# Kernel optimization log

Measured on AMD Instinct MI355X. Metric: run time of the kernel, lower is better.

Reference implementation:

```python
import jax, jax.numpy as jnp
import numpy as np

B = 32          # graphs per batch
NPG = 512       # nodes per graph
EPG = 2048      # original edges per graph (stored in y[:, -1])
N = B * NPG     # 16384 nodes
E = B * EPG     # 65536 edges
GF = 5          # num_global_features
ETOT = E + N    # edges after add_self_loops

def _lin(k, o, i):
    return jax.random.normal(k, (o, i), jnp.float32) / np.sqrt(i)

def setup_inputs():
    key = jax.random.key(0)
    ks = jax.random.split(key, 20)
    x = jax.random.normal(ks[0], (N,), jnp.float32)
    off = (jnp.arange(B, dtype=jnp.int32) * NPG)[:, None]
    src = (jax.random.randint(ks[1], (B, EPG), 0, NPG, dtype=jnp.int32) + off).reshape(-1)
    dst = (jax.random.randint(ks[2], (B, EPG), 0, NPG, dtype=jnp.int32) + off).reshape(-1)
    edge_index = jnp.stack([src, dst])
    edge_attr = jax.random.normal(ks[3], (E, GF), jnp.float32)
    # last global feature = number of edges per graph (module reads y[:, -1])
    y = jax.random.normal(ks[4], (B, GF), jnp.float32).at[:, -1].set(float(EPG)).reshape(-1)
    batch_vector = jnp.repeat(jnp.arange(B, dtype=jnp.int32), NPG)
    p = dict(
        Wn=_lin(ks[5], 512, 1), bn=jnp.zeros(512, jnp.float32),
        We=_lin(ks[6], 511, GF), be=jnp.zeros(511, jnp.float32),
        Wg=_lin(ks[7], 512, GF), bg=jnp.zeros(512, jnp.float32),
        Wl=_lin(ks[8], 1024, 512), bl=jnp.zeros(1024, jnp.float32),
        Wr=_lin(ks[9], 1024, 512), br=jnp.zeros(1024, jnp.float32),
        Wge=_lin(ks[10], 1024, 511),
        att=jax.random.normal(ks[11], (1024,), jnp.float32) / 32.0,
        bgat=jnp.zeros(1024, jnp.float32),
        Wm=_lin(ks[12], 1024, 1024), bm=jnp.zeros(1024, jnp.float32),
        Wmi=_lin(ks[13], 1024, 1024), bmi=jnp.zeros(1024, jnp.float32),
        Wce=_lin(ks[14], 1024, 512), bce=jnp.zeros(1024, jnp.float32),
        W1=_lin(ks[15], 256, 2048), b1=jnp.zeros(256, jnp.float32),
        W2=_lin(ks[16], 1, 256), b2=jnp.zeros(1, jnp.float32),
    )
    return dict(x=x, edge_index=edge_index, edge_attr=edge_attr, y=y,
                batch_vector=batch_vector, **p)

def _leaky(v, s=0.01):
    return jnp.where(v >= 0, v, s * v)

def _forward(edge_index, batch_vector, x, edge_attr, y, Wn, bn, We, be, Wg, bg,
             Wl, bl, Wr, br, Wge, att, bgat, Wm, bm, Wmi, bmi, Wce, bce,
             W1, b1, W2, b2):
    # add_self_loops (fill_value=1.0 for edge_attr), self loops appended last
    loops = jnp.arange(N, dtype=edge_index.dtype)
    src = jnp.concatenate([edge_index[0], loops])
    dst = jnp.concatenate([edge_index[1], loops])
    ea = jnp.concatenate([edge_attr, jnp.ones((N, GF), edge_attr.dtype)], axis=0)
    # preprocessing MLPs (dropout = identity at inference)
    h = _leaky(x[:, None] @ Wn.T + bn)               # [N, 512]
    e = _leaky(ea @ We.T + be)                       # [ETOT, 511]
    yg = _leaky(y.reshape(B, GF) @ Wg.T + bg)        # [B, 512]
    # GATv2Conv, 1 head, concat, negative_slope=0.2, no self-loop add
    xl = h @ Wl.T + bl                               # source transform [N, 1024]
    xr = h @ Wr.T + br                               # target transform [N, 1024]
    m = _leaky(xl[src] + xr[dst] + e @ Wge.T, 0.2)   # [ETOT, 1024]
    logit = m @ att                                  # [ETOT]
    mx = jax.ops.segment_max(logit, dst, num_segments=N)
    ex = jnp.exp(logit - mx[dst])
    alpha = ex / (jax.ops.segment_sum(ex, dst, num_segments=N)[dst] + 1e-16)
    gat = jax.ops.segment_sum(alpha[:, None] * xl[src], dst, num_segments=N) + bgat
    edge_total = jnp.concatenate([e, alpha[:, None]], axis=1)  # [ETOT, 512]
    # GeneralConv: undirected message, add aggregation, identity skip (in==out)
    hm = gat @ Wm.T + bm
    hmi = gat @ Wmi.T + bmi
    eh = edge_total @ Wce.T + bce                    # [ETOT, 1024]
    deg = jax.ops.segment_sum(jnp.ones((ETOT,), gat.dtype), dst, num_segments=N)
    conv = (jax.ops.segment_sum(hm[src] + eh, dst, num_segments=N)
            + deg[:, None] * hmi + gat)              # [N, 1024]
    # global mean pooling (nodes) and module's contiguous edge batch vector
    nc = jax.ops.segment_sum(jnp.ones((N,), conv.dtype), batch_vector, num_segments=B)
    pn = jax.ops.segment_sum(conv, batch_vector, num_segments=B) / nc[:, None]
    ebatch = jnp.repeat(jnp.arange(B, dtype=jnp.int32), EPG + NPG)
    pe = jax.ops.segment_sum(edge_total, ebatch, num_segments=B) / float(EPG + NPG)
    pooled = jnp.concatenate([pn, pe, yg], axis=1)   # [B, 2048]
    out = _leaky(pooled @ W1.T + b1) @ W2.T + b2
    return jax.nn.sigmoid(out)                       # [B, 1]

def reference(x, edge_index, edge_attr, y, batch_vector, Wn, bn, We, be, Wg, bg,
              Wl, bl, Wr, br, Wge, att, bgat, Wm, bm, Wmi, bmi, Wce, bce,
              W1, b1, W2, b2):
    return _forward(edge_index, batch_vector, x, edge_attr, y, Wn, bn, We, be,
                    Wg, bg, Wl, bl, Wr, br, Wge, att, bgat, Wm, bm, Wmi, bmi,
                    Wce, bce, W1, b1, W2, b2)
```

## Files before the change

### kernel.cpp

```cpp
#include <hip/hip_runtime.h>
#include <cstdint>
#include <cstddef>

#define N_NODES 16384
#define N_EDGES 65536
#define ETOT    81920
#define B_GR    32

typedef __attribute__((ext_vector_type(8))) short bf16x8;
typedef __attribute__((ext_vector_type(4))) float f32x4;

static constexpr size_t OFF_XL    = 0;
static constexpr size_t OFF_XR    = 33554432ULL;
static constexpr size_t OFF_EBF   = 67108864ULL;
static constexpr size_t OFF_HBF   = 67108864ULL;
static constexpr size_t OFF_WCAT  = 83886080ULL;
static constexpr size_t OFF_ROWP  = 67108864ULL;
static constexpr size_t OFF_CSR   = 67174656ULL;
static constexpr size_t OFF_ALPHA = 67502336ULL;
static constexpr size_t OFF_WGEP  = 134217728ULL;
static constexpr size_t OFF_LPART = 135266304ULL;
static constexpr size_t OFF_DEG   = 137363456ULL;
static constexpr size_t OFF_ODEG  = 137428992ULL;
static constexpr size_t OFF_CURS  = 137494528ULL;
static constexpr size_t OFF_PG    = 137560064ULL;
static constexpr size_t OFF_PDG   = 137691136ULL;
static constexpr size_t OFF_PGAT  = 137822208ULL;
static constexpr size_t OFF_PS    = 137953280ULL;
static constexpr size_t OFF_PE    = 138018816ULL;
static constexpr size_t OFF_WLOOP = 138084352ULL;
static constexpr size_t OFF_YG    = 138088448ULL;
static constexpr size_t OFF_PN    = 138153984ULL;

__device__ __forceinline__ float leaky01(float v){ return v >= 0.f ? v : 0.01f*v; }
__device__ __forceinline__ float leaky02(float v){ return v >= 0.f ? v : 0.2f*v; }
__device__ __forceinline__ unsigned short f2bf(float f){
  union { float f; unsigned u; } v; v.f = f;
  unsigned r = v.u + 0x7FFFu + ((v.u >> 16) & 1u);
  return (unsigned short)(r >> 16);
}
__device__ __forceinline__ float bf2f(unsigned short h){
  union { unsigned u; float f; } v; v.u = ((unsigned)h) << 16;
  return v.f;
}

__global__ __launch_bounds__(256) void k_prep0(
    const float* __restrict__ x, const float* __restrict__ Wn, const float* __restrict__ bn,
    const float* __restrict__ Wl, const float* __restrict__ Wr,
    const float* __restrict__ Wge, const float* __restrict__ y,
    const float* __restrict__ Wg, const float* __restrict__ bg,
    const float* __restrict__ We, const float* __restrict__ be,
    float* __restrict__ zone, unsigned short* __restrict__ h_bf,
    unsigned short* __restrict__ Wcat, unsigned short* __restrict__ Wge_p,
    float* __restrict__ yg, float* __restrict__ we_loop) {
  __shared__ float e_lds[512];
  int bx = blockIdx.x, tid = threadIdx.x;
  if (bx < 176) {
    ((float4*)zone)[bx*256 + tid] = (float4){0.f,0.f,0.f,0.f};
  } else if (bx < 1200) {
    int gid = (bx-176)*256 + tid;
    int base = gid*8;
    int n = base >> 9, j = base & 511;
    float xv = x[n];
    float4 w0 = *(const float4*)(Wn + j);
    float4 w1 = *(const float4*)(Wn + j + 4);
    float4 b0 = *(const float4*)(bn + j);
    float4 b1 = *(const float4*)(bn + j + 4);
    unsigned short o[8];
    o[0]=f2bf(leaky01(xv*w0.x+b0.x)); o[1]=f2bf(leaky01(xv*w0.y+b0.y));
    o[2]=f2bf(leaky01(xv*w0.z+b0.z)); o[3]=f2bf(leaky01(xv*w0.w+b0.w));
    o[4]=f2bf(leaky01(xv*w1.x+b1.x)); o[5]=f2bf(leaky01(xv*w1.y+b1.y));
    o[6]=f2bf(leaky01(xv*w1.z+b1.z)); o[7]=f2bf(leaky01(xv*w1.w+b1.w));
    ((uint4*)h_bf)[gid] = *(const uint4*)o;
  } else if (bx < 2224) {
    int i = (bx-1200)*256 + tid;
    int base = i*4;
    const float* src = (base < 524288) ? (Wl + base) : (Wr + base - 524288);
    float4 v = *(const float4*)src;
    ushort4 o; o.x=f2bf(v.x); o.y=f2bf(v.y); o.z=f2bf(v.z); o.w=f2bf(v.w);
    ((ushort4*)Wcat)[i] = o;
  } else if (bx < 4272) {
    int gid = (bx-2224)*256 + tid;
    int j = gid >> 9, k = gid & 511;
    Wge_p[gid] = (k < 511) ? f2bf(Wge[(size_t)j*511 + k]) : (unsigned short)0;
  } else if (bx < 4336) {
    int gid = (bx-4272)*256 + tid;
    int b = gid >> 9, j = gid & 511;
    float s = bg[j];
    #pragma unroll
    for (int k=0;k<5;k++) s += y[b*5+k]*Wg[j*5+k];
    yg[gid] = leaky01(s);
  } else {
    for (int c = tid; c < 512; c += 256) {
      float v = 0.f;
      if (c < 511) {
        float s = be[c];
        #pragma unroll
        for (int q=0;q<5;q++) s += We[c*5+q];
        v = leaky01(s);
      }
      e_lds[c] = v;
    }
    __syncthreads();
    int j = (bx-4336)*256 + tid;
    float s = 0.f;
    for (int k=0;k<511;k++) s += e_lds[k]*Wge[(size_t)j*511+k];
    we_loop[j] = s;
  }
}

__global__ __launch_bounds__(256) void k_prep_e(
    const float* __restrict__ ea, const float* __restrict__ We, const float* __restrict__ be,
    unsigned short* __restrict__ E_bf) {
  int gid = blockIdx.x*256 + threadIdx.x;
  int e = gid >> 6, cg = gid & 63;
  int c0 = cg*8;
  const float* e5 = ea + (size_t)e*5;
  float a0=e5[0], a1=e5[1], a2=e5[2], a3=e5[3], a4=e5[4];
  unsigned short o[8];
  #pragma unroll
  for (int j=0;j<8;j++) {
    int c = c0 + j;
    float v = 0.f;
    if (c < 511) {
      const float* w = We + c*5;
      float s = be[c] + a0*w[0] + a1*w[1] + a2*w[2] + a3*w[3] + a4*w[4];
      v = leaky01(s);
    }
    o[j] = f2bf(v);
  }
  ((uint4*)E_bf)[gid] = *(const uint4*)o;
}

__global__ void k_deg(const int* __restrict__ ei, int* __restrict__ deg, int* __restrict__ odeg) {
  int i = blockIdx.x*blockDim.x + threadIdx.x;
  int s, d;
  if (i < N_EDGES) { s = ei[i]; d = ei[N_EDGES + i]; }
  else { s = i - N_EDGES; d = s; }
  atomicAdd(&deg[d], 1);
  atomicAdd(&odeg[s], 1);
}

__global__ __launch_bounds__(1024) void k_scan(const int* __restrict__ deg, int* __restrict__ rowptr) {
  __shared__ int sums[1024];
  int t = threadIdx.x;
  int local[16]; int s = 0;
  #pragma unroll
  for (int i=0;i<16;i++){ local[i] = deg[t*16+i]; s += local[i]; }
  sums[t] = s; __syncthreads();
  for (int off=1; off<1024; off<<=1) {
    int v = (t >= off) ? sums[t-off] : 0;
    __syncthreads();
    sums[t] += v;
    __syncthreads();
  }
  int run = (t==0) ? 0 : sums[t-1];
  if (t==0) rowptr[0] = 0;
  #pragma unroll
  for (int i=0;i<16;i++){ run += local[i]; rowptr[t*16+i+1] = run; }
}

__global__ void k_fill_csr(const int* __restrict__ ei, const int* __restrict__ rowptr,
                           int* __restrict__ cursor, int* __restrict__ csr) {
  int i = blockIdx.x*blockDim.x + threadIdx.x;
  int d = (i < N_EDGES) ? ei[N_EDGES + i] : (i - N_EDGES);
  int pos = rowptr[d] + atomicAdd(&cursor[d], 1);
  csr[pos] = i;
}


__global__ __launch_bounds__(256) void k_gemm_xlxr(
    const unsigned short* __restrict__ h_bf, const unsigned short* __restrict__ Wcat,
    const float* __restrict__ bl, const float* __restrict__ br,
    unsigned short* __restrict__ xl_bf, unsigned short* __restrict__ xr_bf) {
  __shared__ unsigned short As[2][4096];
  __shared__ unsigned short Bs[2][4096];
  int blk = blockIdx.x;
  int xcd = blk & 7, slot = blk >> 3;
  int bx = xcd*16 + (slot >> 4), by = slot & 15;
  int row0 = bx*128, col0 = by*128;
  int tid = threadIdx.x;
  int w = tid >> 6, lane = tid & 63;
  int wm = w >> 1, wn = w & 1;
  int quad = lane >> 4, l16 = lane & 15;
  int ldoff = w*512 + lane*8;
  const unsigned short* gA = h_bf + (size_t)(row0 + w*16 + l16)*512 + quad*8;
  const unsigned short* gB = Wcat + (size_t)(col0 + w*16 + l16)*512 + quad*8;
  f32x4 acc[4][4];
  #pragma unroll
  for (int i=0;i<4;i++)
    #pragma unroll
    for (int j=0;j<4;j++) acc[i][j] = (f32x4){0.f,0.f,0.f,0.f};

  {
    uint4 a0 = *(const uint4*)(gA);
    uint4 a1 = *(const uint4*)(gA + 32768);
    uint4 b0 = *(const uint4*)(gB);
    uint4 b1 = *(const uint4*)(gB + 32768);
    *(uint4*)&As[0][ldoff] = a0; *(uint4*)&As[0][2048+ldoff] = a1;
    *(uint4*)&Bs[0][ldoff] = b0; *(uint4*)&Bs[0][2048+ldoff] = b1;
  }
  __syncthreads();
  int cur = 0;
  #pragma unroll 2
  for (int k0 = 32; k0 <= 512; k0 += 32) {
    uint4 na0, na1, nb0, nb1;
    bool more = (k0 < 512);
    if (more) {
      na0 = *(const uint4*)(gA + k0);
      na1 = *(const uint4*)(gA + 32768 + k0);
      nb0 = *(const uint4*)(gB + k0);
      nb1 = *(const uint4*)(gB + 32768 + k0);
    }
    bf16x8 af[4], bfr[4];
    #pragma unroll
    for (int mi=0;mi<4;mi++)
      af[mi] = *(const bf16x8*)&As[cur][(wm*4+mi)*512 + quad*128 + l16*8];
    #pragma unroll
    for (int ni=0;ni<4;ni++)
      bfr[ni] = *(const bf16x8*)&Bs[cur][(wn*4+ni)*512 + quad*128 + l16*8];
    #pragma unroll
    for (int mi=0;mi<4;mi++)
      #pragma unroll
      for (int ni=0;ni<4;ni++)
        acc[mi][ni] = __builtin_amdgcn_mfma_f32_16x16x32_bf16(af[mi], bfr[ni], acc[mi][ni], 0, 0, 0);
    if (more) {
      *(uint4*)&As[cur^1][ldoff] = na0; *(uint4*)&As[cur^1][2048+ldoff] = na1;
      *(uint4*)&Bs[cur^1][ldoff] = nb0; *(uint4*)&Bs[cur^1][2048+ldoff] = nb1;
    }
    __syncthreads();
    cur ^= 1;
  }
  bool isL = (by < 8);
  const float* bias = isL ? bl : br;
  unsigned short* O = isL ? xl_bf : xr_bf;
  int cb = isL ? col0 : (col0 - 1024);
  float bias4[4];
  #pragma unroll
  for (int ni=0;ni<4;ni++) bias4[ni] = bias[cb + wn*64 + ni*16 + l16];
  #pragma unroll
  for (int mi=0;mi<4;mi++)
    #pragma unroll
    for (int ni=0;ni<4;ni++) {
      int col = cb + wn*64 + ni*16 + l16;
      #pragma unroll
      for (int r=0;r<4;r++) {
        int row = row0 + wm*64 + mi*16 + quad*4 + r;
        O[(size_t)row*1024 + col] = f2bf(acc[mi][ni][r] + bias4[ni]);
      }
    }
}

__global__ __launch_bounds__(256) void k_mfma_we(
    const unsigned short* __restrict__ E_bf, const unsigned short* __restrict__ Wge_bf,
    const int* __restrict__ ei,
    const unsigned short* __restrict__ xl_bf, const unsigned short* __restrict__ xr_bf,
    const float* __restrict__ att, float* __restrict__ logit_part) {
  __shared__ unsigned short As[2][4096];
  __shared__ unsigned short Bs[2][4096];
  __shared__ float tmp[128];
  int blk = blockIdx.x;
  int xcd = blk & 7, slot = blk >> 3;
  int bx = xcd*64 + (slot >> 3), by = slot & 7;
  int row0 = bx*128, col0 = by*128;
  int tid = threadIdx.x;
  int w = tid >> 6, lane = tid & 63;
  int wm = w >> 1, wn = w & 1;
  int quad = lane >> 4, l16 = lane & 15;
  int ldoff = w*512 + lane*8;
  const unsigned short* gA = E_bf  + (size_t)(row0 + w*16 + l16)*512 + quad*8;
  const unsigned short* gB = Wge_bf + (size_t)(col0 + w*16 + l16)*512 + quad*8;
  f32x4 acc[4][4];
  #pragma unroll
  for (int i=0;i<4;i++)
    #pragma unroll
    for (int j=0;j<4;j++) acc[i][j] = (f32x4){0.f,0.f,0.f,0.f};

  {
    uint4 a0 = *(const uint4*)(gA);
    uint4 a1 = *(const uint4*)(gA + 32768);
    uint4 b0 = *(const uint4*)(gB);
    uint4 b1 = *(const uint4*)(gB + 32768);
    *(uint4*)&As[0][ldoff] = a0; *(uint4*)&As[0][2048+ldoff] = a1;
    *(uint4*)&Bs[0][ldoff] = b0; *(uint4*)&Bs[0][2048+ldoff] = b1;
  }
  __syncthreads();
  int cur = 0;
  #pragma unroll 2
  for (int k0 = 32; k0 <= 512; k0 += 32) {
    uint4 na0, na1, nb0, nb1;
    bool more = (k0 < 512);
    if (more) {
      na0 = *(const uint4*)(gA + k0);
      na1 = *(const uint4*)(gA + 32768 + k0);
      nb0 = *(const uint4*)(gB + k0);
      nb1 = *(const uint4*)(gB + 32768 + k0);
    }
    bf16x8 af[4], bfr[4];
    #pragma unroll
    for (int mi=0;mi<4;mi++)
      af[mi] = *(const bf16x8*)&As[cur][(wm*4+mi)*512 + quad*128 + l16*8];
    #pragma unroll
    for (int ni=0;ni<4;ni++)
      bfr[ni] = *(const bf16x8*)&Bs[cur][(wn*4+ni)*512 + quad*128 + l16*8];
    #pragma unroll
    for (int mi=0;mi<4;mi++)
      #pragma unroll
      for (int ni=0;ni<4;ni++)
        acc[mi][ni] = __builtin_amdgcn_mfma_f32_16x16x32_bf16(af[mi], bfr[ni], acc[mi][ni], 0, 0, 0);
    if (more) {
      *(uint4*)&As[cur^1][ldoff] = na0; *(uint4*)&As[cur^1][2048+ldoff] = na1;
      *(uint4*)&Bs[cur^1][ldoff] = nb0; *(uint4*)&Bs[cur^1][2048+ldoff] = nb1;
    }
    __syncthreads();
    cur ^= 1;
  }
  float att4[4];
  #pragma unroll
  for (int ni=0;ni<4;ni++) att4[ni] = att[col0 + wn*64 + ni*16 + l16];
  float pv[4][4];
  #pragma unroll
  for (int mi=0;mi<4;mi++) {
    #pragma unroll
    for (int r=0;r<4;r++) {
      int e = row0 + wm*64 + mi*16 + quad*4 + r;
      int s = ei[e], d = ei[N_EDGES + e];
      const unsigned short* xlr = xl_bf + (size_t)s*1024;
      const unsigned short* xrr = xr_bf + (size_t)d*1024;
      float p = 0.f;
      #pragma unroll
      for (int ni=0;ni<4;ni++) {
        int col = col0 + wn*64 + ni*16 + l16;
        float z = acc[mi][ni][r] + bf2f(xlr[col]) + bf2f(xrr[col]);
        z = leaky02(z);
        p += z*att4[ni];
      }
      p += __shfl_down(p, 8, 16);
      p += __shfl_down(p, 4, 16);
      p += __shfl_down(p, 2, 16);
      p += __shfl_down(p, 1, 16);
      pv[mi][r] = p;
    }
  }
  if (wn == 1 && l16 == 0) {
    #pragma unroll
    for (int mi=0;mi<4;mi++)
      #pragma unroll
      for (int r=0;r<4;r++)
        tmp[wm*64 + mi*16 + quad*4 + r] = pv[mi][r];
  }
  __syncthreads();
  if (wn == 0 && l16 == 0) {
    #pragma unroll
    for (int mi=0;mi<4;mi++)
      #pragma unroll
      for (int r=0;r<4;r++) {
        int le = wm*64 + mi*16 + quad*4 + r;
        logit_part[(size_t)(row0 + le)*8 + by] = pv[mi][r] + tmp[le];
      }
  }
}

__global__ __launch_bounds__(256) void k_softmax_gat(
    const int* __restrict__ ei, const int* __restrict__ rowptr, const int* __restrict__ csr,
    const float* __restrict__ logit_part,
    const unsigned short* __restrict__ xl_bf, const unsigned short* __restrict__ xr_bf,
    const float* __restrict__ we_loop, const float* __restrict__ att,
    const float* __restrict__ bgat,
    float* __restrict__ alpha, unsigned short* __restrict__ gat_bf) {
  __shared__ float sl[256];
  __shared__ int   se[256];
  __shared__ float red[256];
  int blk = blockIdx.x;
  int n = ((blk & 7) << 11) + (blk >> 3);
  int tid = threadIdx.x;
  {
    ushort4 a = ((const ushort4*)(xl_bf + (size_t)n*1024))[tid];
    ushort4 b = ((const ushort4*)(xr_bf + (size_t)n*1024))[tid];
    float4 c = ((const float4*)we_loop)[tid];
    float4 t = ((const float4*)att)[tid];
    float s = 0.f;
    s += leaky02(bf2f(a.x)+bf2f(b.x)+c.x)*t.x;
    s += leaky02(bf2f(a.y)+bf2f(b.y)+c.y)*t.y;
    s += leaky02(bf2f(a.z)+bf2f(b.z)+c.z)*t.z;
    s += leaky02(bf2f(a.w)+bf2f(b.w)+c.w)*t.w;
    red[tid] = s;
  }
  __syncthreads();
  #pragma unroll
  for (int off=128; off; off>>=1){ if (tid<off) red[tid] += red[tid+off]; __syncthreads(); }
  float sll = red[0];
  __syncthreads();

  int beg = rowptr[n], end = rowptr[n+1], cnt = end - beg;
  float m = -1e30f;
  for (int p = beg+tid; p < end; p += 256) {
    int e = csr[p];
    float lg;
    if (e < N_EDGES) {
      const float4* lp = (const float4*)(logit_part + (size_t)e*8);
      float4 q0 = lp[0], q1 = lp[1];
      lg = q0.x+q0.y+q0.z+q0.w+q1.x+q1.y+q1.z+q1.w;
    } else lg = sll;
    int idx = p - beg;
    if (idx < 256) { se[idx] = e; sl[idx] = lg; }
    m = fmaxf(m, lg);
  }
  red[tid] = m; __syncthreads();
  #pragma unroll
  for (int off=128; off; off>>=1){ if (tid<off) red[tid] = fmaxf(red[tid], red[tid+off]); __syncthreads(); }
  m = red[0];
  __syncthreads();
  float ss = 0.f;
  for (int p = beg+tid; p < end; p += 256) {
    int idx = p - beg;
    ss += expf(sl[idx] - m);
  }
  red[tid] = ss; __syncthreads();
  #pragma unroll
  for (int off=128; off; off>>=1){ if (tid<off) red[tid] += red[tid+off]; __syncthreads(); }
  float inv = 1.f/(red[0] + 1e-16f);
  __syncthreads();
  for (int p = beg+tid; p < end; p += 256) {
    int idx = p - beg;
    float a = expf(sl[idx] - m)*inv;
    alpha[se[idx]] = a;
    sl[idx] = a;
  }
  __syncthreads();
  float4 acc = ((const float4*)bgat)[tid];
  for (int p = 0; p < cnt; p++) {
    float a = sl[p]; int e = se[p];
    int s = (e < N_EDGES) ? ei[e] : (e - N_EDGES);
    ushort4 v = ((const ushort4*)(xl_bf + (size_t)s*1024))[tid];
    acc.x += a*bf2f(v.x); acc.y += a*bf2f(v.y); acc.z += a*bf2f(v.z); acc.w += a*bf2f(v.w);
  }
  ushort4 o; o.x=f2bf(acc.x); o.y=f2bf(acc.y); o.z=f2bf(acc.z); o.w=f2bf(acc.w);
  ((ushort4*)(gat_bf + (size_t)n*1024))[tid] = o;
}

__global__ __launch_bounds__(256) void k_nodepool(
    const unsigned short* __restrict__ gat_bf, const int* __restrict__ odeg,
    const int* __restrict__ rowptr,
    float* __restrict__ P_G, float* __restrict__ P_DG, float* __restrict__ P_gat) {
  int b = blockIdx.x, yy = blockIdx.y;
  int nc = yy >> 2, cg = yy & 3;
  int col = cg*256 + threadIdx.x;
  float a1=0.f, a2=0.f, a3=0.f;
  int n0 = b*512 + nc*128;
  for (int i=0;i<128;i++){
    int n = n0 + i;
    float g = bf2f(gat_bf[(size_t)n*1024 + col]);
    float od = (float)odeg[n];
    float dg = (float)(rowptr[n+1]-rowptr[n]);
    a1 += od*g; a2 += dg*g; a3 += g;
  }
  atomicAdd(&P_G[b*1024+col], a1);
  atomicAdd(&P_DG[b*1024+col], a2);
  atomicAdd(&P_gat[b*1024+col], a3);
}

__global__ __launch_bounds__(256) void k_edgepool(
    const float* __restrict__ ea, const float* __restrict__ We, const float* __restrict__ be,
    const float* __restrict__ alpha, float* __restrict__ P_S, float* __restrict__ pe) {
  __shared__ float sea[640];
  __shared__ float sal[128];
  int b = blockIdx.x, chy = blockIdx.y, tid = threadIdx.x;
  int mode = (chy < 20) ? 0 : 1;
  int ch = (chy < 20) ? chy : (chy - 20);
  int c1 = tid, c2 = tid + 256;
  bool v2 = (c2 < 511);
  float w1[5], w2[5]={0,0,0,0,0}, b1v, b2v=0.f;
  #pragma unroll
  for (int q=0;q<5;q++) w1[q] = We[c1*5+q];
  b1v = be[c1];
  if (v2) {
    #pragma unroll
    for (int q=0;q<5;q++) w2[q] = We[c2*5+q];
    b2v = be[c2];
  }
  int base = (mode == 0)
    ? ((ch < 16) ? (b*2048 + ch*128) : (N_EDGES + b*512 + (ch-16)*128))
    : (b*2560 + ch*128);
  for (int i=tid;i<640;i+=256){
    int r = base + i/5;
    sea[i] = (r < N_EDGES) ? ea[(size_t)r*5 + (i%5)] : 1.0f;
  }
  for (int i=tid;i<128;i+=256) sal[i] = alpha[base + i];
  __syncthreads();
  float acc1 = 0.f, acc2 = 0.f;
  for (int rr=0; rr<128; rr++) {
    const float* er = &sea[rr*5];
    acc1 += leaky01(b1v + er[0]*w1[0]+er[1]*w1[1]+er[2]*w1[2]+er[3]*w1[3]+er[4]*w1[4]);
    if (v2) acc2 += leaky01(b2v + er[0]*w2[0]+er[1]*w2[1]+er[2]*w2[2]+er[3]*w2[3]+er[4]*w2[4]);
    else    acc2 += sal[rr];
  }
  if (mode == 0) {
    atomicAdd(&P_S[b*512+c1], acc1);
    atomicAdd(&P_S[b*512+c2], acc2);
  } else {
    const float sc = 1.f/2560.f;
    atomicAdd(&pe[b*512+c1], acc1*sc);
    atomicAdd(&pe[b*512+c2], acc2*sc);
  }
}

__global__ __launch_bounds__(256) void k_pn(
    const float* __restrict__ P_G, const float* __restrict__ P_DG,
    const float* __restrict__ P_S, const float* __restrict__ P_gat,
    const float* __restrict__ Wm, const float* __restrict__ bm,
    const float* __restrict__ Wmi, const float* __restrict__ bmi,
    const float* __restrict__ Wce, const float* __restrict__ bce,
    float* __restrict__ pn) {
  __shared__ float sPg[1024], sPdg[1024], sPs[512];
  int b = blockIdx.x, col0 = blockIdx.y*64;
  int tid = threadIdx.x, w = tid >> 6, lane = tid & 63;
  for (int i=tid;i<1024;i+=256){ sPg[i]=P_G[b*1024+i]; sPdg[i]=P_DG[b*1024+i]; }
  for (int i=tid;i<512;i+=256) sPs[i]=P_S[b*512+i];
  __syncthreads();
  for (int c=0;c<16;c++){
    int j = col0 + w*16 + c;
    const float* wm  = Wm  + (size_t)j*1024;
    const float* wmi = Wmi + (size_t)j*1024;
    const float* wce = Wce + (size_t)j*512;
    float s = 0.f;
    #pragma unroll 4
    for (int i=0;i<16;i++){ int k = lane + i*64; s += sPg[k]*wm[k] + sPdg[k]*wmi[k]; }
    #pragma unroll 4
    for (int i=0;i<8;i++){ int k = lane + i*64; s += sPs[k]*wce[k]; }
    #pragma unroll
    for (int off=32; off; off>>=1) s += __shfl_down(s, off);
    if (lane == 0) {
      pn[b*1024+j] = (s + P_gat[b*1024+j] + 2560.f*(bm[j]+bmi[j]+bce[j])) * (1.f/512.f);
    }
  }
}

__global__ __launch_bounds__(256) void k_final(
    const float* __restrict__ pn, const float* __restrict__ pe, const float* __restrict__ yg,
    const float* __restrict__ W1, const float* __restrict__ b1,
    const float* __restrict__ W2, const float* __restrict__ b2,
    float* __restrict__ out) {
  __shared__ float pooled[2048];
  __shared__ float red[256];
  int b = blockIdx.x, tid = threadIdx.x;
  for (int i=tid;i<1024;i+=256) pooled[i]      = pn[b*1024+i];
  for (int i=tid;i<512;i+=256)  pooled[1024+i] = pe[b*512+i];
  for (int i=tid;i<512;i+=256)  pooled[1536+i] = yg[b*512+i];
  __syncthreads();
  const float4* w4 = (const float4*)(W1 + (size_t)tid*2048);
  const float4* p4 = (const float4*)pooled;
  float s = b1[tid];
  for (int k=0;k<512;k++){
    float4 w = w4[k]; float4 p = p4[k];
    s += w.x*p.x + w.y*p.y + w.z*p.z + w.w*p.w;
  }
  s = leaky01(s);
  red[tid] = s * W2[tid];
  __syncthreads();
  for (int off=128; off; off>>=1){
    if (tid < off) red[tid] += red[tid+off];
    __syncthreads();
  }
  if (tid == 0){
    float o = red[0] + b2[0];
    out[b] = 1.f/(1.f+expf(-o));
  }
}

extern "C" void kernel_launch(void* const* d_in, const int* in_sizes, int n_in,
                              void* d_out, int out_size, void* d_ws, size_t ws_size,
                              hipStream_t stream) {
  const float* x   = (const float*)d_in[0];
  const int*   ei  = (const int*)  d_in[1];
  const float* ea  = (const float*)d_in[2];
  const float* y   = (const float*)d_in[3];
  const float* Wn  = (const float*)d_in[5];
  const float* bn  = (const float*)d_in[6];
  const float* We  = (const float*)d_in[7];
  const float* be  = (const float*)d_in[8];
  const float* Wg  = (const float*)d_in[9];
  const float* bg  = (const float*)d_in[10];
  const float* Wl  = (const float*)d_in[11];
  const float* bl  = (const float*)d_in[12];
  const float* Wr  = (const float*)d_in[13];
  const float* br  = (const float*)d_in[14];
  const float* Wge = (const float*)d_in[15];
  const float* att = (const float*)d_in[16];
  const float* bgat= (const float*)d_in[17];
  const float* Wm  = (const float*)d_in[18];
  const float* bm  = (const float*)d_in[19];
  const float* Wmi = (const float*)d_in[20];
  const float* bmi = (const float*)d_in[21];
  const float* Wce = (const float*)d_in[22];
  const float* bce = (const float*)d_in[23];
  const float* W1  = (const float*)d_in[24];
  const float* b1  = (const float*)d_in[25];
  const float* W2  = (const float*)d_in[26];
  const float* b2  = (const float*)d_in[27];
  float* out = (float*)d_out;

  char* ws = (char*)d_ws;
  unsigned short* xl_bf  = (unsigned short*)(ws + OFF_XL);
  unsigned short* xr_bf  = (unsigned short*)(ws + OFF_XR);
  unsigned short* gat_bf = (unsigned short*)(ws + OFF_XR);
  unsigned short* E_bf   = (unsigned short*)(ws + OFF_EBF);
  unsigned short* h_bf   = (unsigned short*)(ws + OFF_HBF);
  unsigned short* Wcat   = (unsigned short*)(ws + OFF_WCAT);
  unsigned short* Wge_p  = (unsigned short*)(ws + OFF_WGEP);
  float* lpart  = (float*)(ws + OFF_LPART);
  float* zone   = (float*)(ws + OFF_DEG);
  int*   deg    = (int*)  (ws + OFF_DEG);
  int*   odeg   = (int*)  (ws + OFF_ODEG);
  int*   cursor = (int*)  (ws + OFF_CURS);
  float* P_G    = (float*)(ws + OFF_PG);
  float* P_DG   = (float*)(ws + OFF_PDG);
  float* P_gat  = (float*)(ws + OFF_PGAT);
  float* P_S    = (float*)(ws + OFF_PS);
  float* pe     = (float*)(ws + OFF_PE);
  int*   rowptr = (int*)  (ws + OFF_ROWP);
  int*   csr    = (int*)  (ws + OFF_CSR);
  float* alpha  = (float*)(ws + OFF_ALPHA);
  float* we_loop= (float*)(ws + OFF_WLOOP);
  float* yg     = (float*)(ws + OFF_YG);
  float* pn     = (float*)(ws + OFF_PN);

  k_prep0<<<dim3(4340), dim3(256), 0, stream>>>(x, Wn, bn, Wl, Wr, Wge, y, Wg, bg, We, be,
                                                zone, h_bf, Wcat, Wge_p, yg, we_loop);
  k_gemm_xlxr<<<dim3(2048), dim3(256), 0, stream>>>(h_bf, Wcat, bl, br, xl_bf, xr_bf);
  k_prep_e<<<dim3(16384), dim3(256), 0, stream>>>(ea, We, be, E_bf);
  k_mfma_we<<<dim3(4096), dim3(256), 0, stream>>>(E_bf, Wge_p, ei, xl_bf, xr_bf, att, lpart);
  k_deg<<<dim3(320), dim3(256), 0, stream>>>(ei, deg, odeg);
  k_scan<<<dim3(1), dim3(1024), 0, stream>>>(deg, rowptr);
  k_fill_csr<<<dim3(320), dim3(256), 0, stream>>>(ei, rowptr, cursor, csr);
  k_softmax_gat<<<dim3(16384), dim3(256), 0, stream>>>(ei, rowptr, csr, lpart, xl_bf, xr_bf,
                                                       we_loop, att, bgat, alpha, gat_bf);
  k_nodepool<<<dim3(32,16), dim3(256), 0, stream>>>(gat_bf, odeg, rowptr, P_G, P_DG, P_gat);
  k_edgepool<<<dim3(32,40), dim3(256), 0, stream>>>(ea, We, be, alpha, P_S, pe);
  k_pn<<<dim3(32,16), dim3(256), 0, stream>>>(P_G, P_DG, P_S, P_gat, Wm, bm, Wmi, bmi, Wce, bce, pn);
  k_final<<<dim3(32), dim3(256), 0, stream>>>(pn, pe, yg, W1, b1, W2, b2, out);
}
```

Measured before the change: 617.2 us.

## Load GEMM B operands directly from global and transpose epilogue through LDS

In both MFMA GEMM kernels the weight (B) tile is no longer staged through shared memory. Each wave instead loads its bf16 fragments straight from global memory, relying on the cache since the weights are shared across blocks. This halves LDS use and drops the B shared-memory stores. In k_mfma_we, the attention-logit epilogue now writes the accumulators to LDS in transposed form. Four threads per edge can then read contiguous 32-column spans of xl/xr with 16-byte vector loads instead of scattered 2-byte gathers. The trade-off is unstaged global loads of B inside the inner loop and extra LDS traffic and barriers in the epilogue.

```diff
diff --git a/kernel.cpp b/kernel.cpp
--- a/kernel.cpp
+++ b/kernel.cpp
@@ -174,7 +174,6 @@
     const float* __restrict__ bl, const float* __restrict__ br,
     unsigned short* __restrict__ xl_bf, unsigned short* __restrict__ xr_bf) {
   __shared__ unsigned short As[2][4096];
-  __shared__ unsigned short Bs[2][4096];
   int blk = blockIdx.x;
   int xcd = blk & 7, slot = blk >> 3;
   int bx = xcd*16 + (slot >> 4), by = slot & 15;
@@ -185,7 +184,7 @@
   int quad = lane >> 4, l16 = lane & 15;
   int ldoff = w*512 + lane*8;
   const unsigned short* gA = h_bf + (size_t)(row0 + w*16 + l16)*512 + quad*8;
-  const unsigned short* gB = Wcat + (size_t)(col0 + w*16 + l16)*512 + quad*8;
+  const unsigned short* gB = Wcat + (size_t)(col0 + wn*64 + l16)*512 + quad*8;
   f32x4 acc[4][4];
   #pragma unroll
   for (int i=0;i<4;i++)
@@ -195,30 +194,26 @@
   {
     uint4 a0 = *(const uint4*)(gA);
     uint4 a1 = *(const uint4*)(gA + 32768);
-    uint4 b0 = *(const uint4*)(gB);
-    uint4 b1 = *(const uint4*)(gB + 32768);
     *(uint4*)&As[0][ldoff] = a0; *(uint4*)&As[0][2048+ldoff] = a1;
-    *(uint4*)&Bs[0][ldoff] = b0; *(uint4*)&Bs[0][2048+ldoff] = b1;
   }
   __syncthreads();
   int cur = 0;
   #pragma unroll 2
   for (int k0 = 32; k0 <= 512; k0 += 32) {
-    uint4 na0, na1, nb0, nb1;
+    uint4 na0, na1;
     bool more = (k0 < 512);
     if (more) {
       na0 = *(const uint4*)(gA + k0);
       na1 = *(const uint4*)(gA + 32768 + k0);
-      nb0 = *(const uint4*)(gB + k0);
-      nb1 = *(const uint4*)(gB + 32768 + k0);
-    }
-    bf16x8 af[4], bfr[4];
+    }
+    bf16x8 bfr[4];
+    #pragma unroll
+    for (int ni=0;ni<4;ni++)
+      bfr[ni] = *(const bf16x8*)(gB + (size_t)ni*8192 + (k0 - 32));
+    bf16x8 af[4];
     #pragma unroll
     for (int mi=0;mi<4;mi++)
       af[mi] = *(const bf16x8*)&As[cur][(wm*4+mi)*512 + quad*128 + l16*8];
-    #pragma unroll
-    for (int ni=0;ni<4;ni++)
-      bfr[ni] = *(const bf16x8*)&Bs[cur][(wn*4+ni)*512 + quad*128 + l16*8];
     #pragma unroll
     for (int mi=0;mi<4;mi++)
       #pragma unroll
@@ -226,7 +221,6 @@
         acc[mi][ni] = __builtin_amdgcn_mfma_f32_16x16x32_bf16(af[mi], bfr[ni], acc[mi][ni], 0, 0, 0);
     if (more) {
       *(uint4*)&As[cur^1][ldoff] = na0; *(uint4*)&As[cur^1][2048+ldoff] = na1;
-      *(uint4*)&Bs[cur^1][ldoff] = nb0; *(uint4*)&Bs[cur^1][2048+ldoff] = nb1;
     }
     __syncthreads();
     cur ^= 1;
@@ -256,9 +250,9 @@
     const int* __restrict__ ei,
     const unsigned short* __restrict__ xl_bf, const unsigned short* __restrict__ xr_bf,
     const float* __restrict__ att, float* __restrict__ logit_part) {
-  __shared__ unsigned short As[2][4096];
-  __shared__ unsigned short Bs[2][4096];
-  __shared__ float tmp[128];
+  __shared__ alignas(16) char smem[33280];
+  unsigned short (*As)[4096] = (unsigned short (*)[4096])smem;
+  float* accT = (float*)smem;
   int blk = blockIdx.x;
   int xcd = blk & 7, slot = blk >> 3;
   int bx = xcd*64 + (slot >> 3), by = slot & 7;
@@ -269,7 +263,7 @@
   int quad = lane >> 4, l16 = lane & 15;
   int ldoff = w*512 + lane*8;
   const unsigned short* gA = E_bf  + (size_t)(row0 + w*16 + l16)*512 + quad*8;
-  const unsigned short* gB = Wge_bf + (size_t)(col0 + w*16 + l16)*512 + quad*8;
+  const unsigned short* gB = Wge_bf + (size_t)(col0 + wn*64 + l16)*512 + quad*8;
   f32x4 acc[4][4];
   #pragma unroll
   for (int i=0;i<4;i++)
@@ -279,30 +273,26 @@
   {
     uint4 a0 = *(const uint4*)(gA);
     uint4 a1 = *(const uint4*)(gA + 32768);
-    uint4 b0 = *(const uint4*)(gB);
-    uint4 b1 = *(const uint4*)(gB + 32768);
     *(uint4*)&As[0][ldoff] = a0; *(uint4*)&As[0][2048+ldoff] = a1;
-    *(uint4*)&Bs[0][ldoff] = b0; *(uint4*)&Bs[0][2048+ldoff] = b1;
   }
   __syncthreads();
   int cur = 0;
   #pragma unroll 2
   for (int k0 = 32; k0 <= 512; k0 += 32) {
-    uint4 na0, na1, nb0, nb1;
+    uint4 na0, na1;
     bool more = (k0 < 512);
     if (more) {
       na0 = *(const uint4*)(gA + k0);
       na1 = *(const uint4*)(gA + 32768 + k0);
-      nb0 = *(const uint4*)(gB + k0);
-      nb1 = *(const uint4*)(gB + 32768 + k0);
-    }
-    bf16x8 af[4], bfr[4];
+    }
+    bf16x8 bfr[4];
+    #pragma unroll
+    for (int ni=0;ni<4;ni++)
+      bfr[ni] = *(const bf16x8*)(gB + (size_t)ni*8192 + (k0 - 32));
+    bf16x8 af[4];
     #pragma unroll
     for (int mi=0;mi<4;mi++)
       af[mi] = *(const bf16x8*)&As[cur][(wm*4+mi)*512 + quad*128 + l16*8];
-    #pragma unroll
-    for (int ni=0;ni<4;ni++)
-      bfr[ni] = *(const bf16x8*)&Bs[cur][(wn*4+ni)*512 + quad*128 + l16*8];
     #pragma unroll
     for (int mi=0;mi<4;mi++)
       #pragma unroll
@@ -310,54 +300,56 @@
         acc[mi][ni] = __builtin_amdgcn_mfma_f32_16x16x32_bf16(af[mi], bfr[ni], acc[mi][ni], 0, 0, 0);
     if (more) {
       *(uint4*)&As[cur^1][ldoff] = na0; *(uint4*)&As[cur^1][2048+ldoff] = na1;
-      *(uint4*)&Bs[cur^1][ldoff] = nb0; *(uint4*)&Bs[cur^1][2048+ldoff] = nb1;
     }
     __syncthreads();
     cur ^= 1;
   }
-  float att4[4];
-  #pragma unroll
-  for (int ni=0;ni<4;ni++) att4[ni] = att[col0 + wn*64 + ni*16 + l16];
-  float pv[4][4];
-  #pragma unroll
-  for (int mi=0;mi<4;mi++) {
-    #pragma unroll
-    for (int r=0;r<4;r++) {
-      int e = row0 + wm*64 + mi*16 + quad*4 + r;
-      int s = ei[e], d = ei[N_EDGES + e];
-      const unsigned short* xlr = xl_bf + (size_t)s*1024;
-      const unsigned short* xrr = xr_bf + (size_t)d*1024;
-      float p = 0.f;
+  int e_loc = tid >> 2, cq = tid & 3;
+  #pragma unroll
+  for (int eh = 0; eh < 2; eh++) {
+    if (wm == eh) {
       #pragma unroll
-      for (int ni=0;ni<4;ni++) {
-        int col = col0 + wn*64 + ni*16 + l16;
-        float z = acc[mi][ni][r] + bf2f(xlr[col]) + bf2f(xrr[col]);
-        z = leaky02(z);
-        p += z*att4[ni];
-      }
-      p += __shfl_down(p, 8, 16);
-      p += __shfl_down(p, 4, 16);
-      p += __shfl_down(p, 2, 16);
-      p += __shfl_down(p, 1, 16);
-      pv[mi][r] = p;
-    }
-  }
-  if (wn == 1 && l16 == 0) {
-    #pragma unroll
-    for (int mi=0;mi<4;mi++)
-      #pragma unroll
-      for (int r=0;r<4;r++)
-        tmp[wm*64 + mi*16 + quad*4 + r] = pv[mi][r];
-  }
-  __syncthreads();
-  if (wn == 0 && l16 == 0) {
-    #pragma unroll
-    for (int mi=0;mi<4;mi++)
-      #pragma unroll
-      for (int r=0;r<4;r++) {
-        int le = wm*64 + mi*16 + quad*4 + r;
-        logit_part[(size_t)(row0 + le)*8 + by] = pv[mi][r] + tmp[le];
-      }
+      for (int mi=0;mi<4;mi++)
+        #pragma unroll
+        for (int ni=0;ni<4;ni++) {
+          int colb = wn*64 + ni*16 + l16;
+          #pragma unroll
+          for (int r=0;r<4;r++)
+            accT[(mi*16 + quad*4 + r)*130 + colb] = acc[mi][ni][r];
+        }
+    }
+    __syncthreads();
+    int e = row0 + eh*64 + e_loc;
+    int s = ei[e], d = ei[N_EDGES + e];
+    const uint4* xlp = (const uint4*)(xl_bf + (size_t)s*1024 + col0 + cq*32);
+    const uint4* xrp = (const uint4*)(xr_bf + (size_t)d*1024 + col0 + cq*32);
+    const float* accrow = accT + e_loc*130 + cq*32;
+    const float* attp = att + col0 + cq*32;
+    float p = 0.f;
+    #pragma unroll
+    for (int g=0; g<4; g++) {
+      uint4 xa = xlp[g];
+      uint4 xb = xrp[g];
+      float4 at0 = *(const float4*)(attp + g*8);
+      float4 at1 = *(const float4*)(attp + g*8 + 4);
+      float4 ac0 = *(const float4*)(accrow + g*8);
+      float4 ac1 = *(const float4*)(accrow + g*8 + 4);
+      const unsigned short* ua = (const unsigned short*)&xa;
+      const unsigned short* ub = (const unsigned short*)&xb;
+      float z;
+      z = ac0.x + bf2f(ua[0]) + bf2f(ub[0]); z = leaky02(z); p += z*at0.x;
+      z = ac0.y + bf2f(ua[1]) + bf2f(ub[1]); z = leaky02(z); p += z*at0.y;
+      z = ac0.z + bf2f(ua[2]) + bf2f(ub[2]); z = leaky02(z); p += z*at0.z;
+      z = ac0.w + bf2f(ua[3]) + bf2f(ub[3]); z = leaky02(z); p += z*at0.w;
+      z = ac1.x + bf2f(ua[4]) + bf2f(ub[4]); z = leaky02(z); p += z*at1.x;
+      z = ac1.y + bf2f(ua[5]) + bf2f(ub[5]); z = leaky02(z); p += z*at1.y;
+      z = ac1.z + bf2f(ua[6]) + bf2f(ub[6]); z = leaky02(z); p += z*at1.z;
+      z = ac1.w + bf2f(ua[7]) + bf2f(ub[7]); z = leaky02(z); p += z*at1.w;
+    }
+    p += __shfl_down(p, 2, 4);
+    p += __shfl_down(p, 1, 4);
+    if (cq == 0) logit_part[(size_t)e*8 + by] = p;
+    __syncthreads();
   }
 }
 
```

Result: slower. 733.8 us (+18.9%).
